# Optimization experiments

Hardware: AMD Instinct MI355X
Metric: run time of the kernel (lower is better)

The kernel has to match this reference:

```python
import jax, jax.numpy as jnp
import numpy as np

B, C, H, W = 512, 1, 280, 280
KS, S, P_PAD, F = 28, 28, 0, 16
HS = (H - KS + 2 * P_PAD) // S + 1  # 10
WS = (W - KS + 2 * P_PAD) // S + 1  # 10
P = HS * WS                          # 100 patches
OUT = 10


def setup_inputs() -> dict:
    key = jax.random.key(0)
    k1, k2, k3, k4, k5 = jax.random.split(key, 5)
    x = jax.random.normal(k1, (B, C, H, W), dtype=jnp.float32)
    weight = jax.random.normal(k2, (P * F, C, KS, KS), dtype=jnp.float32) * 0.05
    bias = jax.random.normal(k3, (P * F, C), dtype=jnp.float32) * 0.05
    dec_w = jax.random.normal(k4, (OUT, P * F * C), dtype=jnp.float32) * 0.05
    dec_b = jax.random.normal(k5, (OUT,), dtype=jnp.float32) * 0.05
    return {"x": x, "weight": weight, "bias": bias, "dec_w": dec_w, "dec_b": dec_b}


def _extract_patches(x):
    # x: (B, C, H+2p, W+2p) -> (B, P, C, KS, KS), patch order: row-major over (hs, ws)
    rows = jnp.arange(HS)[:, None] * S + jnp.arange(KS)[None, :]  # (HS, KS)
    cols = jnp.arange(WS)[:, None] * S + jnp.arange(KS)[None, :]  # (WS, KS)
    p = x[:, :, rows, :]            # (B, C, HS, KS, W)
    p = p[:, :, :, :, cols]         # (B, C, HS, KS, WS, KS)
    p = p.transpose(0, 2, 4, 1, 3, 5)  # (B, HS, WS, C, KS, KS)
    return p.reshape(B, P, C, KS, KS)


def reference(x, weight, bias, dec_w, dec_b):
    xp = jnp.pad(x, ((0, 0), (0, 0), (P_PAD, P_PAD), (P_PAD, P_PAD)))
    patches = _extract_patches(xp)                       # (B, P, C, KS, KS)
    # torch: x.repeat(1, f, ...) tiles patches f times; weight flat index i -> (f_idx, p_idx)
    w = weight.reshape(F, P, C, KS, KS)
    y = jnp.einsum('bpckl,fpckl->bfpc', patches, w)      # (B, F, P, C)
    y = y + bias.reshape(F, P, C)
    y = jax.nn.relu(y)
    y = y.reshape(B, F * P * C)
    return y @ dec_w.T + dec_b
```

## Files before the change

### kernel.cpp

```cpp
#include <hip/hip_runtime.h>
#include <stdint.h>

#define BATCH 512
#define HWIMG 78400
#define WROW  280
#define PNUM  100
#define FNUM  16
#define ONUM  10

__global__ __launch_bounds__(256) void init_out(const float* __restrict__ dec_b,
                                                float* __restrict__ out) {
    int i = blockIdx.x * 256 + threadIdx.x;
    if (i < BATCH * ONUM) out[i] = dec_b[i % ONUM];
}

__global__ __launch_bounds__(64, 4) void lcn_direct(
    const float* __restrict__ x,
    const float* __restrict__ weight,
    const float* __restrict__ bias,
    const float* __restrict__ dec_w,
    float* __restrict__ out)
{
    const int t  = threadIdx.x;
    const int kg = t & 7;
    const int fg = (t >> 3) & 3;
    const int bg = t >> 5;
    const int bx = blockIdx.x;
    const int p    = bx >> 5;
    const int bgrp = bx & 31;
    const int b0   = bgrp * 16;
    const int pr = p / 10, pc = p % 10;
    const int kge = (kg < 7) ? kg : 0;

    const float* xb[8];
#pragma unroll
    for (int i = 0; i < 8; ++i)
        xb[i] = x + (size_t)(b0 + bg * 8 + i) * HWIMG
                  + (size_t)(pr * 28) * WROW + pc * 28 + kge * 4;
    const float* wb[4];
#pragma unroll
    for (int j = 0; j < 4; ++j)
        wb[j] = weight + (size_t)((fg * 4 + j) * PNUM + p) * 784 + kge * 4;

    float acc[8][4];
#pragma unroll
    for (int i = 0; i < 8; ++i)
#pragma unroll
        for (int j = 0; j < 4; ++j) acc[i][j] = 0.f;

#pragma unroll 1
    for (int c = 0; c < 7; ++c) {
#pragma unroll
        for (int m = 0; m < 4; ++m) {
            float4 wv[4];
#pragma unroll
            for (int j = 0; j < 4; ++j)
                wv[j] = *reinterpret_cast<const float4*>(wb[j] + m * 28);
#pragma unroll
            for (int i = 0; i < 8; ++i) {
                float4 av = *reinterpret_cast<const float4*>(xb[i] + m * WROW);
#pragma unroll
                for (int j = 0; j < 4; ++j) {
                    acc[i][j] = fmaf(av.x, wv[j].x, acc[i][j]);
                    acc[i][j] = fmaf(av.y, wv[j].y, acc[i][j]);
                    acc[i][j] = fmaf(av.z, wv[j].z, acc[i][j]);
                    acc[i][j] = fmaf(av.w, wv[j].w, acc[i][j]);
                }
            }
        }
#pragma unroll
        for (int i = 0; i < 8; ++i) xb[i] += 4 * WROW;
#pragma unroll
        for (int j = 0; j < 4; ++j) wb[j] += 4 * 28;
    }

    const float km = (kg < 7) ? 1.f : 0.f;
#pragma unroll
    for (int i = 0; i < 8; ++i)
#pragma unroll
        for (int j = 0; j < 4; ++j) acc[i][j] *= km;

#pragma unroll
    for (int d = 1; d < 8; d <<= 1)
#pragma unroll
        for (int i = 0; i < 8; ++i)
#pragma unroll
            for (int j = 0; j < 4; ++j)
                acc[i][j] += __shfl_xor(acc[i][j], d, 64);

    float y[8][4];
#pragma unroll
    for (int j = 0; j < 4; ++j) {
        const float bs = bias[(fg * 4 + j) * PNUM + p];
#pragma unroll
        for (int i = 0; i < 8; ++i) {
            float v = acc[i][j] + bs;
            y[i][j] = v > 0.f ? v : 0.f;
        }
    }

    float po[8][2];
    const int  o0  = kg * 2;
    const bool act = (kg < 5);
    if (act) {
        float dwv[4][2];
#pragma unroll
        for (int j = 0; j < 4; ++j)
#pragma unroll
            for (int oo = 0; oo < 2; ++oo)
                dwv[j][oo] = dec_w[(size_t)(o0 + oo) * (PNUM * FNUM) + (fg * 4 + j) * PNUM + p];
#pragma unroll
        for (int i = 0; i < 8; ++i)
#pragma unroll
            for (int oo = 0; oo < 2; ++oo) {
                float s = 0.f;
#pragma unroll
                for (int j = 0; j < 4; ++j) s = fmaf(y[i][j], dwv[j][oo], s);
                po[i][oo] = s;
            }
    } else {
#pragma unroll
        for (int i = 0; i < 8; ++i) { po[i][0] = 0.f; po[i][1] = 0.f; }
    }

#pragma unroll
    for (int d = 8; d < 32; d <<= 1)
#pragma unroll
        for (int i = 0; i < 8; ++i)
#pragma unroll
            for (int oo = 0; oo < 2; ++oo)
                po[i][oo] += __shfl_xor(po[i][oo], d, 64);

    if (act && fg == 0) {
#pragma unroll
        for (int i = 0; i < 8; ++i)
#pragma unroll
            for (int oo = 0; oo < 2; ++oo)
                atomicAdd(&out[(size_t)(b0 + bg * 8 + i) * ONUM + o0 + oo], po[i][oo]);
    }
}

extern "C" void kernel_launch(void* const* d_in, const int* in_sizes, int n_in,
                              void* d_out, int out_size, void* d_ws, size_t ws_size,
                              hipStream_t stream) {
    const float* x     = (const float*)d_in[0];
    const float* w     = (const float*)d_in[1];
    const float* bias  = (const float*)d_in[2];
    const float* dec_w = (const float*)d_in[3];
    const float* dec_b = (const float*)d_in[4];
    float* out = (float*)d_out;

    init_out<<<(BATCH * ONUM + 255) / 256, 256, 0, stream>>>(dec_b, out);
    lcn_direct<<<(BATCH / 16) * PNUM, 64, 0, stream>>>(x, w, bias, dec_w, out);
}
```

Baseline: 260.1 us.

## Stage patch rows via async global-to-LDS double buffering across five patches

Each block now covers 16 batch images and five adjacent patches of one patch row, and runs 256 threads instead of 64. Input rows and weights are streamed into double-buffered shared memory with global_load_lds, synchronised by explicit waitcnt and barriers. Computation reads float4s from LDS, and the decoder partial sums are accumulated across the five patches before the atomic adds. The goal is contiguous 560-byte row loads, overlap of memory traffic with FMA, and fewer atomics, at the cost of a barrier per row and more shared-memory pressure.

New measurement: 671.8 us. 2.58x slower.

```diff
diff --git a/kernel.cpp b/kernel.cpp
--- a/kernel.cpp
+++ b/kernel.cpp
@@ -8,135 +8,185 @@
 #define FNUM  16
 #define ONUM  10
 
+typedef __attribute__((address_space(1))) const void cg_void;
+typedef __attribute__((address_space(3))) void lds_void;
+
 __global__ __launch_bounds__(256) void init_out(const float* __restrict__ dec_b,
                                                 float* __restrict__ out) {
     int i = blockIdx.x * 256 + threadIdx.x;
     if (i < BATCH * ONUM) out[i] = dec_b[i % ONUM];
 }
 
-__global__ __launch_bounds__(64, 4) void lcn_direct(
+__global__ __launch_bounds__(256, 4) void lcn_rows(
     const float* __restrict__ x,
     const float* __restrict__ weight,
     const float* __restrict__ bias,
     const float* __restrict__ dec_w,
     float* __restrict__ out)
 {
+    __shared__ float4 lx[2][616];
+    __shared__ float4 lw[2][616];
+
     const int t  = threadIdx.x;
     const int kg = t & 7;
     const int fg = (t >> 3) & 3;
     const int bg = t >> 5;
-    const int bx = blockIdx.x;
-    const int p    = bx >> 5;
-    const int bgrp = bx & 31;
+    const int wid = t >> 6;
+    const int ln  = t & 63;
+
+    const int bx   = blockIdx.x;
+    const int pent = bx & 1;
+    const int bgrp = (bx >> 1) & 31;
+    const int pr   = bx >> 6;
     const int b0   = bgrp * 16;
-    const int pr = p / 10, pc = p % 10;
-    const int kge = (kg < 7) ? kg : 0;
-
-    const float* xb[8];
-#pragma unroll
-    for (int i = 0; i < 8; ++i)
-        xb[i] = x + (size_t)(b0 + bg * 8 + i) * HWIMG
-                  + (size_t)(pr * 28) * WROW + pc * 28 + kge * 4;
-    const float* wb[4];
-#pragma unroll
-    for (int j = 0; j < 4; ++j)
-        wb[j] = weight + (size_t)((fg * 4 + j) * PNUM + p) * 784 + kge * 4;
-
-    float acc[8][4];
-#pragma unroll
-    for (int i = 0; i < 8; ++i)
-#pragma unroll
-        for (int j = 0; j < 4; ++j) acc[i][j] = 0.f;
+    const int kge  = (kg < 7) ? kg : 0;
+
+    const float* xsrc[3];
+    const float* wsrc[3];
+#pragma unroll
+    for (int k = 0; k < 3; ++k) {
+        int gi = wid * 140 + k * 64 + ln;
+        if (gi > 559) gi = 559;
+        const int b   = gi / 35;
+        const int off = gi % 35;
+        xsrc[k] = x + (size_t)(b0 + b) * HWIMG + (size_t)(pr * 28) * WROW
+                    + pent * 140 + off * 4;
+        const int seg = gi / 7;
+        const int o7  = gi % 7;
+        const int f   = seg / 5;
+        const int pcl = seg % 5;
+        const int p   = pr * 10 + pent * 5 + pcl;
+        wsrc[k] = weight + (size_t)(f * PNUM + p) * 784 + o7 * 4;
+    }
+
+    auto issue = [&](int bb) {
+#pragma unroll
+        for (int k = 0; k < 3; ++k)
+            __builtin_amdgcn_global_load_lds((cg_void*)xsrc[k],
+                (lds_void*)&lx[bb][wid * 140 + k * 64 + ln], 16, 0, 0);
+#pragma unroll
+        for (int k = 0; k < 3; ++k)
+            __builtin_amdgcn_global_load_lds((cg_void*)wsrc[k],
+                (lds_void*)&lw[bb][wid * 140 + k * 64 + ln], 16, 0, 0);
+#pragma unroll
+        for (int k = 0; k < 3; ++k) { xsrc[k] += WROW; wsrc[k] += 28; }
+    };
+
+    float acc[5][2][4];
+#pragma unroll
+    for (int pc = 0; pc < 5; ++pc)
+#pragma unroll
+        for (int i = 0; i < 2; ++i)
+#pragma unroll
+            for (int j = 0; j < 4; ++j) acc[pc][i][j] = 0.f;
+
+    issue(0);
+    issue(1);
 
 #pragma unroll 1
-    for (int c = 0; c < 7; ++c) {
-#pragma unroll
-        for (int m = 0; m < 4; ++m) {
-            float4 wv[4];
+    for (int c = 0; c < 28; ++c) {
+        const int buf = c & 1;
+        if (c < 27) asm volatile("s_waitcnt vmcnt(6)" ::: "memory");
+        else        asm volatile("s_waitcnt vmcnt(0)" ::: "memory");
+        __builtin_amdgcn_s_barrier();
+        asm volatile("" ::: "memory");
+
+#pragma unroll
+        for (int pc = 0; pc < 5; ++pc) {
+            float4 wvv[4];
 #pragma unroll
             for (int j = 0; j < 4; ++j)
-                wv[j] = *reinterpret_cast<const float4*>(wb[j] + m * 28);
-#pragma unroll
-            for (int i = 0; i < 8; ++i) {
-                float4 av = *reinterpret_cast<const float4*>(xb[i] + m * WROW);
+                wvv[j] = lw[buf][((fg * 4 + j) * 5 + pc) * 7 + kge];
+#pragma unroll
+            for (int i = 0; i < 2; ++i) {
+                const float4 av = lx[buf][(bg * 2 + i) * 35 + pc * 7 + kge];
 #pragma unroll
                 for (int j = 0; j < 4; ++j) {
-                    acc[i][j] = fmaf(av.x, wv[j].x, acc[i][j]);
-                    acc[i][j] = fmaf(av.y, wv[j].y, acc[i][j]);
-                    acc[i][j] = fmaf(av.z, wv[j].z, acc[i][j]);
-                    acc[i][j] = fmaf(av.w, wv[j].w, acc[i][j]);
+                    acc[pc][i][j] = fmaf(av.x, wvv[j].x, acc[pc][i][j]);
+                    acc[pc][i][j] = fmaf(av.y, wvv[j].y, acc[pc][i][j]);
+                    acc[pc][i][j] = fmaf(av.z, wvv[j].z, acc[pc][i][j]);
+                    acc[pc][i][j] = fmaf(av.w, wvv[j].w, acc[pc][i][j]);
                 }
             }
         }
-#pragma unroll
-        for (int i = 0; i < 8; ++i) xb[i] += 4 * WROW;
-#pragma unroll
-        for (int j = 0; j < 4; ++j) wb[j] += 4 * 28;
+
+        asm volatile("" ::: "memory");
+        __builtin_amdgcn_s_barrier();
+        if (c + 2 < 28) issue(buf);
     }
 
     const float km = (kg < 7) ? 1.f : 0.f;
 #pragma unroll
-    for (int i = 0; i < 8; ++i)
-#pragma unroll
-        for (int j = 0; j < 4; ++j) acc[i][j] *= km;
+    for (int pc = 0; pc < 5; ++pc)
+#pragma unroll
+        for (int i = 0; i < 2; ++i)
+#pragma unroll
+            for (int j = 0; j < 4; ++j) acc[pc][i][j] *= km;
 
 #pragma unroll
     for (int d = 1; d < 8; d <<= 1)
 #pragma unroll
-        for (int i = 0; i < 8; ++i)
-#pragma unroll
-            for (int j = 0; j < 4; ++j)
-                acc[i][j] += __shfl_xor(acc[i][j], d, 64);
-
-    float y[8][4];
-#pragma unroll
-    for (int j = 0; j < 4; ++j) {
-        const float bs = bias[(fg * 4 + j) * PNUM + p];
-#pragma unroll
-        for (int i = 0; i < 8; ++i) {
-            float v = acc[i][j] + bs;
-            y[i][j] = v > 0.f ? v : 0.f;
+        for (int pc = 0; pc < 5; ++pc)
+#pragma unroll
+            for (int i = 0; i < 2; ++i)
+#pragma unroll
+                for (int j = 0; j < 4; ++j)
+                    acc[pc][i][j] += __shfl_xor(acc[pc][i][j], d, 64);
+
+#pragma unroll
+    for (int pc = 0; pc < 5; ++pc) {
+        const int p = pr * 10 + pent * 5 + pc;
+#pragma unroll
+        for (int j = 0; j < 4; ++j) {
+            const float bs = bias[(fg * 4 + j) * PNUM + p];
+#pragma unroll
+            for (int i = 0; i < 2; ++i) {
+                float v = acc[pc][i][j] + bs;
+                acc[pc][i][j] = v > 0.f ? v : 0.f;
+            }
         }
     }
 
-    float po[8][2];
+    float po[2][2];
     const int  o0  = kg * 2;
     const bool act = (kg < 5);
     if (act) {
-        float dwv[4][2];
-#pragma unroll
-        for (int j = 0; j < 4; ++j)
-#pragma unroll
-            for (int oo = 0; oo < 2; ++oo)
-                dwv[j][oo] = dec_w[(size_t)(o0 + oo) * (PNUM * FNUM) + (fg * 4 + j) * PNUM + p];
-#pragma unroll
-        for (int i = 0; i < 8; ++i)
-#pragma unroll
-            for (int oo = 0; oo < 2; ++oo) {
-                float s = 0.f;
-#pragma unroll
-                for (int j = 0; j < 4; ++j) s = fmaf(y[i][j], dwv[j][oo], s);
-                po[i][oo] = s;
+#pragma unroll
+        for (int i = 0; i < 2; ++i) { po[i][0] = 0.f; po[i][1] = 0.f; }
+#pragma unroll
+        for (int pc = 0; pc < 5; ++pc) {
+            const int p = pr * 10 + pent * 5 + pc;
+#pragma unroll
+            for (int j = 0; j < 4; ++j) {
+                const int fidx = (fg * 4 + j) * PNUM + p;
+#pragma unroll
+                for (int oo = 0; oo < 2; ++oo) {
+                    const float dw = dec_w[(size_t)(o0 + oo) * (PNUM * FNUM) + fidx];
+#pragma unroll
+                    for (int i = 0; i < 2; ++i)
+                        po[i][oo] = fmaf(acc[pc][i][j], dw, po[i][oo]);
+                }
             }
+        }
     } else {
 #pragma unroll
-        for (int i = 0; i < 8; ++i) { po[i][0] = 0.f; po[i][1] = 0.f; }
+        for (int i = 0; i < 2; ++i) { po[i][0] = 0.f; po[i][1] = 0.f; }
     }
 
 #pragma unroll
     for (int d = 8; d < 32; d <<= 1)
 #pragma unroll
-        for (int i = 0; i < 8; ++i)
+        for (int i = 0; i < 2; ++i)
 #pragma unroll
             for (int oo = 0; oo < 2; ++oo)
                 po[i][oo] += __shfl_xor(po[i][oo], d, 64);
 
     if (act && fg == 0) {
 #pragma unroll
-        for (int i = 0; i < 8; ++i)
+        for (int i = 0; i < 2; ++i)
 #pragma unroll
             for (int oo = 0; oo < 2; ++oo)
-                atomicAdd(&out[(size_t)(b0 + bg * 8 + i) * ONUM + o0 + oo], po[i][oo]);
+                atomicAdd(&out[(size_t)(b0 + bg * 2 + i) * ONUM + o0 + oo], po[i][oo]);
     }
 }
 
@@ -151,5 +201,5 @@
     float* out = (float*)d_out;
 
     init_out<<<(BATCH * ONUM + 255) / 256, 256, 0, stream>>>(dec_b, out);
-    lcn_direct<<<(BATCH / 16) * PNUM, 64, 0, stream>>>(x, w, bias, dec_w, out);
+    lcn_rows<<<(BATCH / 16) * PNUM / 5, 256, 0, stream>>>(x, w, bias, dec_w, out);
 }
```
